# Optimization experiments

Measured on AMD Instinct MI355X. Metric: run time of the kernel, lower is better.

The kernel has to match this reference:

```python
import jax, jax.numpy as jnp
import numpy as np

HIDDEN = 450
DEPTH = 6
ATOM_FDIM = 35          # len(ELEM_LIST)+6+5+1
BOND_FDIM = 5
MAX_NB = 15
N_ATOMS = 20000
N_BONDS = 40000
N_MESS = 16000          # tree messages (row 0 is the zero padding slot)
N_MOLS = 1000


def _linear_init(key, out_dim, in_dim):
    s = 1.0 / np.sqrt(in_dim)
    return jax.random.uniform(key, (out_dim, in_dim), jnp.float32, -s, s)


def setup_inputs() -> dict:
    key = jax.random.key(0)
    ks = jax.random.split(key, 9)
    total_msg = N_MESS + N_BONDS
    fatoms = jax.random.normal(ks[0], (N_ATOMS, ATOM_FDIM), jnp.float32)
    fbonds = jax.random.normal(ks[1], (N_BONDS, ATOM_FDIM + BOND_FDIM), jnp.float32)
    agraph = jax.random.randint(ks[2], (N_ATOMS, MAX_NB), 0, total_msg, jnp.int32)
    bgraph = jax.random.randint(ks[3], (N_BONDS, MAX_NB), 0, total_msg, jnp.int32)
    tree_message = jax.random.normal(ks[4], (N_MESS, HIDDEN), jnp.float32)
    tree_message = tree_message.at[0].set(0.0)  # index 0 = padding message
    # uniform scope: N_MOLS molecules of N_ATOMS//N_MOLS atoms each
    mol_ids = jnp.repeat(jnp.arange(N_MOLS, dtype=jnp.int32), N_ATOMS // N_MOLS)
    W_i = _linear_init(ks[5], HIDDEN, ATOM_FDIM + BOND_FDIM)
    W_h = _linear_init(ks[6], HIDDEN, HIDDEN)
    W_o = _linear_init(ks[7], HIDDEN, ATOM_FDIM + HIDDEN)
    s = 1.0 / np.sqrt(ATOM_FDIM + HIDDEN)
    b_o = jax.random.uniform(ks[8], (HIDDEN,), jnp.float32, -s, s)
    return {"fatoms": fatoms, "fbonds": fbonds, "agraph": agraph, "bgraph": bgraph,
            "mol_ids": mol_ids, "n_mols": N_MOLS, "tree_message": tree_message,
            "W_i": W_i, "W_h": W_h, "W_o": W_o, "b_o": b_o}


def reference(fatoms, fbonds, agraph, bgraph, mol_ids, n_mols, tree_message,
              W_i, W_h, W_o, b_o):
    binput = fbonds @ W_i.T                       # [B, H]
    graph_message = jax.nn.relu(binput)
    for _ in range(DEPTH - 1):                    # static depth loop
        message = jnp.concatenate([tree_message, graph_message], axis=0)  # [M+B, H]
        nei_message = message[bgraph].sum(axis=1)  # gather [B, MAX_NB, H] -> [B, H]
        graph_message = jax.nn.relu(binput + nei_message @ W_h.T)
    message = jnp.concatenate([tree_message, graph_message], axis=0)
    nei_message = message[agraph].sum(axis=1)      # [A, H]
    ainput = jnp.concatenate([fatoms, nei_message], axis=1)  # [A, ATOM_FDIM+H]
    atom_hiddens = jax.nn.relu(ainput @ W_o.T + b_o)          # [A, H]
    # mean over each molecule's atoms (scope)
    sums = jax.ops.segment_sum(atom_hiddens, mol_ids, num_segments=n_mols)
    counts = jax.ops.segment_sum(jnp.ones((atom_hiddens.shape[0], 1), atom_hiddens.dtype),
                                 mol_ids, num_segments=n_mols)
    return sums / counts
```

## Files before the change

### kernel.cpp

```cpp
#include <hip/hip_runtime.h>

#define HIDDEN 450
#define MAX_NB 15
#define N_ATOMS 20000
#define N_BONDS 40000
#define N_MESS  16000
#define N_MOLS  1000
#define KPAD    512
#define MSTRIDE 456

typedef unsigned int uint;
typedef unsigned short ushort;
typedef __bf16 bf16x8 __attribute__((ext_vector_type(8)));
typedef float  f32x4  __attribute__((ext_vector_type(4)));

__device__ __forceinline__ ushort f2bf(float f) {
    uint u = __builtin_bit_cast(uint, f);
    u += 0x7fffu + ((u >> 16) & 1u);
    return (ushort)(u >> 16);
}
__device__ __forceinline__ float bfhi(uint w) {
    return __builtin_bit_cast(float, w & 0xffff0000u);
}
__device__ __forceinline__ float bflo(uint w) {
    return __builtin_bit_cast(float, w << 16);
}


__global__ __launch_bounds__(256) void pack_tree(const float* __restrict__ tree,
                                                 ushort* __restrict__ tbuf) {
    const int r = blockIdx.x, t = threadIdx.x;
    if (t < 228) {
        uint p = 0;
        if (t < 225) {
            const float2 v = *(const float2*)&tree[(size_t)r * HIDDEN + 2 * t];
            p = (uint)f2bf(v.x) | ((uint)f2bf(v.y) << 16);
        }
        ((uint*)(tbuf + (size_t)r * MSTRIDE))[t] = p;
    }
}

__global__ __launch_bounds__(256) void pack_bonds(const float* __restrict__ fbonds,
                                                  ushort* __restrict__ Abuf) {
    const int r = blockIdx.x * 4 + (threadIdx.x >> 6);
    const int t = threadIdx.x & 63;
    if (r >= N_BONDS) return;
    ushort* row = Abuf + (size_t)r * KPAD;
    if (t < 40) row[t] = f2bf(fbonds[(size_t)r * 40 + t]);
    else        row[t] = 0;
    if (t < 16) row[496 + t] = 0;
}

__global__ __launch_bounds__(256) void pack_atoms(const float* __restrict__ fatoms,
                                                  ushort* __restrict__ Aout) {
    const int r = blockIdx.x * 4 + (threadIdx.x >> 6);
    const int t = threadIdx.x & 63;
    if (r >= N_ATOMS) return;
    ushort* row = Aout + (size_t)r * KPAD;
    if (t < 40) row[t] = (t < 35) ? f2bf(fatoms[(size_t)r * 35 + t]) : (ushort)0;
    if (t < 16) row[496 + t] = 0;
}

__global__ __launch_bounds__(256) void pack_w(const float* __restrict__ W_i,
                                              const float* __restrict__ W_h,
                                              const float* __restrict__ W_o,
                                              ushort* __restrict__ Wcat,
                                              ushort* __restrict__ Wocat) {
    const int n = blockIdx.x;
    for (int c = threadIdx.x; c < KPAD; c += 256) {
        float v = 0.0f, vo = 0.0f;
        if (n < HIDDEN) {
            if (c < 40)       v = W_i[(size_t)n * 40 + c];
            else if (c < 490) v = W_h[(size_t)n * HIDDEN + (c - 40)];
            if (c < 35)       vo = W_o[(size_t)n * 485 + c];
            else if (c >= 40 && c < 490) vo = W_o[(size_t)n * 485 + 35 + (c - 40)];
        }
        Wcat [(size_t)n * KPAD + c] = f2bf(v);
        Wocat[(size_t)n * KPAD + c] = f2bf(vo);
    }
}

__global__ __launch_bounds__(256) void precompute_base(const int* __restrict__ g,
                                                       const ushort* __restrict__ tbuf,
                                                       ushort* __restrict__ base,
                                                       int nrows) {
    const int r = blockIdx.x * 4 + (threadIdx.x >> 6);
    const int lane = threadIdx.x & 63;
    if (r >= nrows) return;
    const int* gr = g + (size_t)r * MAX_NB;
    int idx[MAX_NB];
#pragma unroll
    for (int j = 0; j < MAX_NB; ++j) idx[j] = gr[j];
    if (lane >= 57) return;
    const int off = lane * 8;
    float acc[8] = {};
#pragma unroll
    for (int j = 0; j < MAX_NB; ++j) {
        if (idx[j] < N_MESS) {
            const uint4 w = *(const uint4*)(tbuf + (size_t)idx[j] * MSTRIDE + off);
            acc[0] += bflo(w.x); acc[1] += bfhi(w.x);
            acc[2] += bflo(w.y); acc[3] += bfhi(w.y);
            acc[4] += bflo(w.z); acc[5] += bfhi(w.z);
            acc[6] += bflo(w.w); acc[7] += bfhi(w.w);
        }
    }
    uint4 p;
    p.x = (uint)f2bf(acc[0]) | ((uint)f2bf(acc[1]) << 16);
    p.y = (uint)f2bf(acc[2]) | ((uint)f2bf(acc[3]) << 16);
    p.z = (uint)f2bf(acc[4]) | ((uint)f2bf(acc[5]) << 16);
    p.w = (uint)f2bf(acc[6]) | ((uint)f2bf(acc[7]) << 16);
    *(uint4*)(base + (size_t)r * MSTRIDE + off) = p;
}

__global__ __launch_bounds__(256) void gather_dyn(const int* __restrict__ g,
                                                  const ushort* __restrict__ base,
                                                  const ushort* __restrict__ gmsg,
                                                  ushort* __restrict__ dst, int nrows) {
    const int r = blockIdx.x * 4 + (threadIdx.x >> 6);
    const int lane = threadIdx.x & 63;
    if (r >= nrows) return;
    const int* gr = g + (size_t)r * MAX_NB;
    int idx[MAX_NB];
#pragma unroll
    for (int j = 0; j < MAX_NB; ++j) idx[j] = gr[j];
    if (lane >= 57) return;
    const int off = lane * 8;
    const uint4 b = *(const uint4*)(base + (size_t)r * MSTRIDE + off);
    float acc[8];
    acc[0] = bflo(b.x); acc[1] = bfhi(b.x);
    acc[2] = bflo(b.y); acc[3] = bfhi(b.y);
    acc[4] = bflo(b.z); acc[5] = bfhi(b.z);
    acc[6] = bflo(b.w); acc[7] = bfhi(b.w);
#pragma unroll
    for (int j = 0; j < MAX_NB; ++j) {
        if (idx[j] >= N_MESS) {
            const uint4 w = *(const uint4*)(gmsg + (size_t)(idx[j] - N_MESS) * MSTRIDE + off);
            acc[0] += bflo(w.x); acc[1] += bfhi(w.x);
            acc[2] += bflo(w.y); acc[3] += bfhi(w.y);
            acc[4] += bflo(w.z); acc[5] += bfhi(w.z);
            acc[6] += bflo(w.w); acc[7] += bfhi(w.w);
        }
    }
    uint4 p;
    p.x = (uint)f2bf(acc[0]) | ((uint)f2bf(acc[1]) << 16);
    p.y = (uint)f2bf(acc[2]) | ((uint)f2bf(acc[3]) << 16);
    p.z = (uint)f2bf(acc[4]) | ((uint)f2bf(acc[5]) << 16);
    p.w = (uint)f2bf(acc[6]) | ((uint)f2bf(acc[7]) << 16);
    *(uint4*)(dst + (size_t)r * KPAD + 40 + off) = p;
}

template <int MODE, int KT>
__global__ __launch_bounds__(256, 2) void mfma_gemm(
    const ushort* __restrict__ A, int M,
    const ushort* __restrict__ W,
    const float* __restrict__ bias, const int* __restrict__ mol_ids,
    ushort* __restrict__ gout, float* __restrict__ aout, int mtiles) {
    __shared__ ushort At[64 * KT * 32];
    const int tid = threadIdx.x;
    const int id  = blockIdx.x;
    const int b     = id & 7;
    const int n_blk = (id >> 3) & 1;
    const int m_blk = (id >> 4) * 8 + b;
    if (m_blk >= mtiles) return;
    const int m0 = m_blk * 64, n0 = n_blk * 256;
    const int CPR = KT * 4;

    {
        const int srow = tid >> 2;
        const int c0   = tid & 3;
        const ushort* gsrc = A + (size_t)min(m0 + srow, M - 1) * KPAD;
        ushort* lrow = At + srow * (KT * 32);
#pragma unroll
        for (int c = c0; c < CPR; c += 4) {
            const uint4 v = *(const uint4*)(gsrc + c * 8);
            *(uint4*)&lrow[(c ^ (srow & 7)) * 8] = v;
        }
    }
    __syncthreads();

    const int lane = tid & 63;
    const int wave = tid >> 6;
    const int wn = wave * 64;
    const int lr = lane & 15;
    const int lk = lane >> 4;

    size_t woff[4];
#pragma unroll
    for (int s = 0; s < 4; ++s)
        woff[s] = (size_t)(n0 + wn + s * 16 + lr) * KPAD + lk * 8;

    f32x4 acc[4][4];
#pragma unroll
    for (int i = 0; i < 4; ++i)
#pragma unroll
        for (int j = 0; j < 4; ++j) acc[i][j] = (f32x4){0.f, 0.f, 0.f, 0.f};

    bf16x8 wa[4], wb[4], afa[4];
#pragma unroll
    for (int s = 0; s < 4; ++s) wa[s] = *(const bf16x8*)&W[woff[s]];
#pragma unroll
    for (int s = 0; s < 4; ++s)
        wb[s] = (KT > 1) ? *(const bf16x8*)&W[woff[s] + 32] : wa[s];
#pragma unroll
    for (int mt = 0; mt < 4; ++mt) {
        const int row = mt * 16 + lr;
        afa[mt] = *(const bf16x8*)&At[(row * CPR + (lk ^ (row & 7))) * 8];
    }

#pragma unroll
    for (int i = 0; i < KT; ++i) {
        bf16x8 wc[4], afb[4];
        if (i + 2 < KT) {
#pragma unroll
            for (int s = 0; s < 4; ++s)
                wc[s] = *(const bf16x8*)&W[woff[s] + (size_t)(i + 2) * 32];
        }
        if (i + 1 < KT) {
#pragma unroll
            for (int mt = 0; mt < 4; ++mt) {
                const int row = mt * 16 + lr;
                const int chunk = (((i + 1) * 4 + lk)) ^ (row & 7);
                afb[mt] = *(const bf16x8*)&At[(row * CPR + chunk) * 8];
            }
        }
#pragma unroll
        for (int mt = 0; mt < 4; ++mt)
#pragma unroll
            for (int nt = 0; nt < 4; ++nt)
                acc[mt][nt] = __builtin_amdgcn_mfma_f32_16x16x32_bf16(
                    afa[mt], wa[nt], acc[mt][nt], 0, 0, 0);
        if (i + 1 < KT) {
#pragma unroll
            for (int s = 0; s < 4; ++s) wa[s] = wb[s];
#pragma unroll
            for (int mt = 0; mt < 4; ++mt) afa[mt] = afb[mt];
        }
        if (i + 2 < KT) {
#pragma unroll
            for (int s = 0; s < 4; ++s) wb[s] = wc[s];
        }
    }

    const int col_l = lane & 15;
    const int rbase = (lane >> 4) * 4;
#pragma unroll
    for (int mt = 0; mt < 4; ++mt) {
        const int mbase = m0 + mt * 16 + rbase;
        int mol[4];
        if (MODE == 1) {
#pragma unroll
            for (int reg = 0; reg < 4; ++reg)
                mol[reg] = mol_ids[min(mbase + reg, M - 1)];
        }
#pragma unroll
        for (int nt = 0; nt < 4; ++nt) {
            const int n = n0 + wn + nt * 16 + col_l;
            if (MODE == 0) {
#pragma unroll
                for (int reg = 0; reg < 4; ++reg) {
                    const int m = mbase + reg;
                    if (m >= M) continue;
                    if (n < HIDDEN)
                        gout[(size_t)m * MSTRIDE + n] = f2bf(fmaxf(acc[mt][nt][reg], 0.0f));
                    else if (n < MSTRIDE)
                        gout[(size_t)m * MSTRIDE + n] = 0;
                }
            } else {
                if (n >= HIDDEN) continue;
                const float bsum = bias[n];
                float run = 0.0f;
                int cur = mol[0];
#pragma unroll
                for (int reg = 0; reg < 4; ++reg) {
                    const float v = (mbase + reg < M)
                        ? fmaxf(acc[mt][nt][reg] + bsum, 0.0f) : 0.0f;
                    if (mol[reg] != cur) {
                        atomicAdd(&aout[(size_t)cur * HIDDEN + n], run);
                        cur = mol[reg];
                        run = 0.0f;
                    }
                    run += v;
                }
                atomicAdd(&aout[(size_t)cur * HIDDEN + n], run);
            }
        }
    }
}

__global__ __launch_bounds__(256) void count_atoms(const int* __restrict__ mol_ids,
                                                   float* __restrict__ counts) {
    const int a = blockIdx.x * 256 + threadIdx.x;
    if (a < N_ATOMS) atomicAdd(&counts[mol_ids[a]], 1.0f);
}
__global__ __launch_bounds__(256) void div_counts(float* __restrict__ out,
                                                  const float* __restrict__ counts) {
    const int i = blockIdx.x * 256 + threadIdx.x;
    if (i < N_MOLS * HIDDEN) out[i] = out[i] / counts[i / HIDDEN];
}

extern "C" void kernel_launch(void* const* d_in, const int* in_sizes, int n_in,
                              void* d_out, int out_size, void* d_ws, size_t ws_size,
                              hipStream_t stream) {
    const float* fatoms  = (const float*)d_in[0];
    const float* fbonds  = (const float*)d_in[1];
    const int*   agraph  = (const int*)d_in[2];
    const int*   bgraph  = (const int*)d_in[3];
    const int*   mol_ids = (const int*)d_in[4];
    const float* tree    = (const float*)d_in[6];
    const float* W_i     = (const float*)d_in[7];
    const float* W_h     = (const float*)d_in[8];
    const float* W_o     = (const float*)d_in[9];
    const float* b_o     = (const float*)d_in[10];
    float* out = (float*)d_out;

    ushort* Abuf   = (ushort*)d_ws;
    ushort* Aout   = Abuf   + (size_t)N_BONDS * KPAD;
    ushort* gmsg   = Aout   + (size_t)N_ATOMS * KPAD;
    ushort* tbuf   = gmsg   + (size_t)N_BONDS * MSTRIDE;
    ushort* Wcat   = tbuf   + (size_t)N_MESS  * MSTRIDE;
    ushort* Wocat  = Wcat   + (size_t)KPAD * KPAD;
    ushort* base_b = Wocat  + (size_t)KPAD * KPAD;
    ushort* base_a = base_b + (size_t)N_BONDS * MSTRIDE;
    float*  counts = (float*)(base_a + (size_t)N_ATOMS * MSTRIDE);

    (void)hipMemsetAsync(d_out, 0, (size_t)N_MOLS * HIDDEN * sizeof(float), stream);
    (void)hipMemsetAsync(counts, 0, N_MOLS * sizeof(float), stream);

    const dim3 blk(256);
    pack_tree <<<N_MESS, blk, 0, stream>>>(tree, tbuf);
    pack_bonds<<<(N_BONDS + 3) / 4, blk, 0, stream>>>(fbonds, Abuf);
    pack_atoms<<<(N_ATOMS + 3) / 4, blk, 0, stream>>>(fatoms, Aout);
    pack_w    <<<KPAD, blk, 0, stream>>>(W_i, W_h, W_o, Wcat, Wocat);
    precompute_base<<<(N_BONDS + 3) / 4, blk, 0, stream>>>(bgraph, tbuf, base_b, N_BONDS);
    precompute_base<<<(N_ATOMS + 3) / 4, blk, 0, stream>>>(agraph, tbuf, base_a, N_ATOMS);

    const int mtB = (N_BONDS + 63) / 64;
    const int mtA = (N_ATOMS + 63) / 64;
    const dim3 gB(((mtB + 7) / 8) * 16);
    const dim3 gA(((mtA + 7) / 8) * 16);

    mfma_gemm<0, 2><<<gB, blk, 0, stream>>>(Abuf, N_BONDS, Wcat,
                                            nullptr, nullptr, gmsg, nullptr, mtB);
    for (int it = 0; it < 5; ++it) {
        gather_dyn<<<(N_BONDS + 3) / 4, blk, 0, stream>>>(bgraph, base_b, gmsg,
                                                          Abuf, N_BONDS);
        mfma_gemm<0, 16><<<gB, blk, 0, stream>>>(Abuf, N_BONDS, Wcat,
                                                 nullptr, nullptr, gmsg, nullptr, mtB);
    }
    gather_dyn<<<(N_ATOMS + 3) / 4, blk, 0, stream>>>(agraph, base_a, gmsg,
                                                      Aout, N_ATOMS);
    mfma_gemm<1, 16><<<gA, blk, 0, stream>>>(Aout, N_ATOMS, Wocat,
                                             b_o, mol_ids, nullptr, out, mtA);

    count_atoms<<<(N_ATOMS + 255) / 256, blk, 0, stream>>>(mol_ids, counts);
    div_counts <<<(N_MOLS * HIDDEN + 255) / 256, blk, 0, stream>>>(out, counts);
}
```

Before: 922.7 us.

## Fuse neighbor gather into GEMM via LDS staging with ping-pong message buffers

Replaces the separate gather kernel plus GEMM per depth step with one fused kernel that gathers and sums neighbor messages directly into shared memory, then runs the MFMA GEMM over the full hidden width in a 512-thread block. Input features are stored in a compact 64-wide buffer instead of being padded into a 512-wide A matrix, and message buffers ping-pong to avoid read/write hazards. This removes the round trip of the gathered activation matrix through global memory and halves launch count, at the cost of larger LDS use (64 KB per block), lower occupancy, and gather latency now serialised before the MFMA phase within each block.

```diff
diff --git a/kernel.cpp b/kernel.cpp
--- a/kernel.cpp
+++ b/kernel.cpp
@@ -8,6 +8,7 @@
 #define N_MOLS  1000
 #define KPAD    512
 #define MSTRIDE 456
+#define FSTRIDE 64
 
 typedef unsigned int uint;
 typedef unsigned short ushort;
@@ -45,10 +46,8 @@
     const int r = blockIdx.x * 4 + (threadIdx.x >> 6);
     const int t = threadIdx.x & 63;
     if (r >= N_BONDS) return;
-    ushort* row = Abuf + (size_t)r * KPAD;
-    if (t < 40) row[t] = f2bf(fbonds[(size_t)r * 40 + t]);
-    else        row[t] = 0;
-    if (t < 16) row[496 + t] = 0;
+    Abuf[(size_t)r * FSTRIDE + t] = (t < 40) ? f2bf(fbonds[(size_t)r * 40 + t])
+                                             : (ushort)0;
 }
 
 __global__ __launch_bounds__(256) void pack_atoms(const float* __restrict__ fatoms,
@@ -56,9 +55,8 @@
     const int r = blockIdx.x * 4 + (threadIdx.x >> 6);
     const int t = threadIdx.x & 63;
     if (r >= N_ATOMS) return;
-    ushort* row = Aout + (size_t)r * KPAD;
-    if (t < 40) row[t] = (t < 35) ? f2bf(fatoms[(size_t)r * 35 + t]) : (ushort)0;
-    if (t < 16) row[496 + t] = 0;
+    Aout[(size_t)r * FSTRIDE + t] = (t < 35) ? f2bf(fatoms[(size_t)r * 35 + t])
+                                             : (ushort)0;
 }
 
 __global__ __launch_bounds__(256) void pack_w(const float* __restrict__ W_i,
@@ -112,49 +110,11 @@
     *(uint4*)(base + (size_t)r * MSTRIDE + off) = p;
 }
 
-__global__ __launch_bounds__(256) void gather_dyn(const int* __restrict__ g,
-                                                  const ushort* __restrict__ base,
-                                                  const ushort* __restrict__ gmsg,
-                                                  ushort* __restrict__ dst, int nrows) {
-    const int r = blockIdx.x * 4 + (threadIdx.x >> 6);
-    const int lane = threadIdx.x & 63;
-    if (r >= nrows) return;
-    const int* gr = g + (size_t)r * MAX_NB;
-    int idx[MAX_NB];
-#pragma unroll
-    for (int j = 0; j < MAX_NB; ++j) idx[j] = gr[j];
-    if (lane >= 57) return;
-    const int off = lane * 8;
-    const uint4 b = *(const uint4*)(base + (size_t)r * MSTRIDE + off);
-    float acc[8];
-    acc[0] = bflo(b.x); acc[1] = bfhi(b.x);
-    acc[2] = bflo(b.y); acc[3] = bfhi(b.y);
-    acc[4] = bflo(b.z); acc[5] = bfhi(b.z);
-    acc[6] = bflo(b.w); acc[7] = bfhi(b.w);
-#pragma unroll
-    for (int j = 0; j < MAX_NB; ++j) {
-        if (idx[j] >= N_MESS) {
-            const uint4 w = *(const uint4*)(gmsg + (size_t)(idx[j] - N_MESS) * MSTRIDE + off);
-            acc[0] += bflo(w.x); acc[1] += bfhi(w.x);
-            acc[2] += bflo(w.y); acc[3] += bfhi(w.y);
-            acc[4] += bflo(w.z); acc[5] += bfhi(w.z);
-            acc[6] += bflo(w.w); acc[7] += bfhi(w.w);
-        }
-    }
-    uint4 p;
-    p.x = (uint)f2bf(acc[0]) | ((uint)f2bf(acc[1]) << 16);
-    p.y = (uint)f2bf(acc[2]) | ((uint)f2bf(acc[3]) << 16);
-    p.z = (uint)f2bf(acc[4]) | ((uint)f2bf(acc[5]) << 16);
-    p.w = (uint)f2bf(acc[6]) | ((uint)f2bf(acc[7]) << 16);
-    *(uint4*)(dst + (size_t)r * KPAD + 40 + off) = p;
-}
-
-template <int MODE, int KT>
-__global__ __launch_bounds__(256, 2) void mfma_gemm(
+template <int KT, int AST>
+__global__ __launch_bounds__(256, 2) void mfma_gemm0(
     const ushort* __restrict__ A, int M,
     const ushort* __restrict__ W,
-    const float* __restrict__ bias, const int* __restrict__ mol_ids,
-    ushort* __restrict__ gout, float* __restrict__ aout, int mtiles) {
+    ushort* __restrict__ gout, int mtiles) {
     __shared__ ushort At[64 * KT * 32];
     const int tid = threadIdx.x;
     const int id  = blockIdx.x;
@@ -168,7 +128,7 @@
     {
         const int srow = tid >> 2;
         const int c0   = tid & 3;
-        const ushort* gsrc = A + (size_t)min(m0 + srow, M - 1) * KPAD;
+        const ushort* gsrc = A + (size_t)min(m0 + srow, M - 1) * AST;
         ushort* lrow = At + srow * (KT * 32);
 #pragma unroll
         for (int c = c0; c < CPR; c += 4) {
@@ -246,6 +206,147 @@
 #pragma unroll
     for (int mt = 0; mt < 4; ++mt) {
         const int mbase = m0 + mt * 16 + rbase;
+#pragma unroll
+        for (int nt = 0; nt < 4; ++nt) {
+            const int n = n0 + wn + nt * 16 + col_l;
+#pragma unroll
+            for (int reg = 0; reg < 4; ++reg) {
+                const int m = mbase + reg;
+                if (m >= M) continue;
+                if (n < HIDDEN)
+                    gout[(size_t)m * MSTRIDE + n] = f2bf(fmaxf(acc[mt][nt][reg], 0.0f));
+                else if (n < MSTRIDE)
+                    gout[(size_t)m * MSTRIDE + n] = 0;
+            }
+        }
+    }
+}
+
+template <int MODE>
+__global__ __launch_bounds__(512, 4) void fused_gg(
+    const int* __restrict__ g,
+    const ushort* __restrict__ base,
+    const ushort* __restrict__ gin,
+    const ushort* __restrict__ feat,
+    const ushort* __restrict__ W,
+    const float* __restrict__ bias, const int* __restrict__ mol_ids,
+    ushort* __restrict__ gout, float* __restrict__ aout, int M) {
+    __shared__ ushort At[64 * KPAD];
+    const int tid  = threadIdx.x;
+    const int lane = tid & 63;
+    const int wave = tid >> 6;
+    const int m0 = blockIdx.x * 64;
+
+#pragma unroll 2
+    for (int rr = 0; rr < 8; ++rr) {
+        const int r = (wave << 3) | rr;
+        const int m = min(m0 + r, M - 1);
+        const int sw = r & 7;
+        ushort* lrow = At + r * KPAD;
+        if (lane < 57) {
+            const int* gr = g + (size_t)m * MAX_NB;
+            int idx[MAX_NB];
+#pragma unroll
+            for (int j = 0; j < MAX_NB; ++j) idx[j] = gr[j];
+            const int off = lane * 8;
+            const uint4 b = *(const uint4*)(base + (size_t)m * MSTRIDE + off);
+            float acc[8];
+            acc[0] = bflo(b.x); acc[1] = bfhi(b.x);
+            acc[2] = bflo(b.y); acc[3] = bfhi(b.y);
+            acc[4] = bflo(b.z); acc[5] = bfhi(b.z);
+            acc[6] = bflo(b.w); acc[7] = bfhi(b.w);
+#pragma unroll
+            for (int j = 0; j < MAX_NB; ++j) {
+                if (idx[j] >= N_MESS) {
+                    const uint4 w = *(const uint4*)(gin +
+                        (size_t)(idx[j] - N_MESS) * MSTRIDE + off);
+                    acc[0] += bflo(w.x); acc[1] += bfhi(w.x);
+                    acc[2] += bflo(w.y); acc[3] += bfhi(w.y);
+                    acc[4] += bflo(w.z); acc[5] += bfhi(w.z);
+                    acc[6] += bflo(w.w); acc[7] += bfhi(w.w);
+                }
+            }
+            uint4 p;
+            p.x = (uint)f2bf(acc[0]) | ((uint)f2bf(acc[1]) << 16);
+            p.y = (uint)f2bf(acc[2]) | ((uint)f2bf(acc[3]) << 16);
+            p.z = (uint)f2bf(acc[4]) | ((uint)f2bf(acc[5]) << 16);
+            p.w = (uint)f2bf(acc[6]) | ((uint)f2bf(acc[7]) << 16);
+            *(uint4*)&lrow[((5 + lane) ^ sw) * 8] = p;
+        } else {
+            const int c = (lane < 62) ? (lane - 57) : lane;
+            uint4 v = (uint4){0u, 0u, 0u, 0u};
+            if (lane < 62)
+                v = *(const uint4*)(feat + (size_t)m * FSTRIDE + (lane - 57) * 8);
+            *(uint4*)&lrow[(c ^ sw) * 8] = v;
+        }
+    }
+    __syncthreads();
+
+    const int wn = wave * 64;
+    const int lr = lane & 15;
+    const int lk = lane >> 4;
+
+    size_t woff[4];
+#pragma unroll
+    for (int s = 0; s < 4; ++s)
+        woff[s] = (size_t)(wn + s * 16 + lr) * KPAD + lk * 8;
+
+    f32x4 acc[4][4];
+#pragma unroll
+    for (int i = 0; i < 4; ++i)
+#pragma unroll
+        for (int j = 0; j < 4; ++j) acc[i][j] = (f32x4){0.f, 0.f, 0.f, 0.f};
+
+    bf16x8 wa[4], wb[4], afa[4];
+#pragma unroll
+    for (int s = 0; s < 4; ++s) wa[s] = *(const bf16x8*)&W[woff[s]];
+#pragma unroll
+    for (int s = 0; s < 4; ++s) wb[s] = *(const bf16x8*)&W[woff[s] + 32];
+#pragma unroll
+    for (int mt = 0; mt < 4; ++mt) {
+        const int row = mt * 16 + lr;
+        afa[mt] = *(const bf16x8*)&At[(row * 64 + (lk ^ (row & 7))) * 8];
+    }
+
+#pragma unroll
+    for (int i = 0; i < 16; ++i) {
+        bf16x8 wc[4], afb[4];
+        if (i + 2 < 16) {
+#pragma unroll
+            for (int s = 0; s < 4; ++s)
+                wc[s] = *(const bf16x8*)&W[woff[s] + (size_t)(i + 2) * 32];
+        }
+        if (i + 1 < 16) {
+#pragma unroll
+            for (int mt = 0; mt < 4; ++mt) {
+                const int row = mt * 16 + lr;
+                const int chunk = (((i + 1) * 4 + lk)) ^ (row & 7);
+                afb[mt] = *(const bf16x8*)&At[(row * 64 + chunk) * 8];
+            }
+        }
+#pragma unroll
+        for (int mt = 0; mt < 4; ++mt)
+#pragma unroll
+            for (int nt = 0; nt < 4; ++nt)
+                acc[mt][nt] = __builtin_amdgcn_mfma_f32_16x16x32_bf16(
+                    afa[mt], wa[nt], acc[mt][nt], 0, 0, 0);
+        if (i + 1 < 16) {
+#pragma unroll
+            for (int s = 0; s < 4; ++s) wa[s] = wb[s];
+#pragma unroll
+            for (int mt = 0; mt < 4; ++mt) afa[mt] = afb[mt];
+        }
+        if (i + 2 < 16) {
+#pragma unroll
+            for (int s = 0; s < 4; ++s) wb[s] = wc[s];
+        }
+    }
+
+    const int col_l = lane & 15;
+    const int rbase = (lane >> 4) * 4;
+#pragma unroll
+    for (int mt = 0; mt < 4; ++mt) {
+        const int mbase = m0 + mt * 16 + rbase;
         int mol[4];
         if (MODE == 1) {
 #pragma unroll
@@ -254,7 +355,7 @@
         }
 #pragma unroll
         for (int nt = 0; nt < 4; ++nt) {
-            const int n = n0 + wn + nt * 16 + col_l;
+            const int n = wn + nt * 16 + col_l;
             if (MODE == 0) {
 #pragma unroll
                 for (int reg = 0; reg < 4; ++reg) {
@@ -314,9 +415,10 @@
     float* out = (float*)d_out;
 
     ushort* Abuf   = (ushort*)d_ws;
-    ushort* Aout   = Abuf   + (size_t)N_BONDS * KPAD;
-    ushort* gmsg   = Aout   + (size_t)N_ATOMS * KPAD;
-    ushort* tbuf   = gmsg   + (size_t)N_BONDS * MSTRIDE;
+    ushort* Aout   = Abuf   + (size_t)N_BONDS * FSTRIDE;
+    ushort* gmsgA  = Aout   + (size_t)N_ATOMS * FSTRIDE;
+    ushort* gmsgB  = gmsgA  + (size_t)N_BONDS * MSTRIDE;
+    ushort* tbuf   = gmsgB  + (size_t)N_BONDS * MSTRIDE;
     ushort* Wcat   = tbuf   + (size_t)N_MESS  * MSTRIDE;
     ushort* Wocat  = Wcat   + (size_t)KPAD * KPAD;
     ushort* base_b = Wocat  + (size_t)KPAD * KPAD;
@@ -336,21 +438,20 @@
 
     const int mtB = (N_BONDS + 63) / 64;
     const int mtA = (N_ATOMS + 63) / 64;
-    const dim3 gB(((mtB + 7) / 8) * 16);
-    const dim3 gA(((mtA + 7) / 8) * 16);
-
-    mfma_gemm<0, 2><<<gB, blk, 0, stream>>>(Abuf, N_BONDS, Wcat,
-                                            nullptr, nullptr, gmsg, nullptr, mtB);
+    const dim3 gB0(((mtB + 7) / 8) * 16);
+
+    mfma_gemm0<2, FSTRIDE><<<gB0, blk, 0, stream>>>(Abuf, N_BONDS, Wcat, gmsgA, mtB);
+
+    ushort* cur = gmsgA;
+    ushort* nxt = gmsgB;
+    const dim3 blk2(512);
     for (int it = 0; it < 5; ++it) {
-        gather_dyn<<<(N_BONDS + 3) / 4, blk, 0, stream>>>(bgraph, base_b, gmsg,
-                                                          Abuf, N_BONDS);
-        mfma_gemm<0, 16><<<gB, blk, 0, stream>>>(Abuf, N_BONDS, Wcat,
-                                                 nullptr, nullptr, gmsg, nullptr, mtB);
-    }
-    gather_dyn<<<(N_ATOMS + 3) / 4, blk, 0, stream>>>(agraph, base_a, gmsg,
-                                                      Aout, N_ATOMS);
-    mfma_gemm<1, 16><<<gA, blk, 0, stream>>>(Aout, N_ATOMS, Wocat,
-                                             b_o, mol_ids, nullptr, out, mtA);
+        fused_gg<0><<<mtB, blk2, 0, stream>>>(bgraph, base_b, cur, Abuf, Wcat,
+                                              nullptr, nullptr, nxt, nullptr, N_BONDS);
+        ushort* t = cur; cur = nxt; nxt = t;
+    }
+    fused_gg<1><<<mtA, blk2, 0, stream>>>(agraph, base_a, cur, Aout, Wocat,
+                                          b_o, mol_ids, nullptr, out, N_ATOMS);
 
     count_atoms<<<(N_ATOMS + 255) / 256, blk, 0, stream>>>(mol_ids, counts);
     div_counts <<<(N_MOLS * HIDDEN + 255) / 256, blk, 0, stream>>>(out, counts);
```

Result: slower. 970.0 us (+5.1%).
